# Performance work log

Hardware: AMD Instinct MI355X
Metric: run time of the kernel (lower is better)

## Reference

```python
import jax, jax.numpy as jnp
import numpy as np

HIDDEN = 1024
HEADS = 16
HEAD_DIM = HIDDEN // HEADS
NEG_INF = -1.0e9


def setup_inputs() -> dict:
    key = jax.random.key(0)
    ks = jax.random.split(key, 9)
    B, S = 4, 2048
    scale = 1.0 / np.sqrt(HIDDEN)
    inp = {
        'query': jax.random.normal(ks[0], (B, S, HIDDEN), dtype=jnp.float32),
        'masks': jnp.ones((B, S), dtype=jnp.float32),
        'Wq': jax.random.normal(ks[1], (HIDDEN, HIDDEN), dtype=jnp.float32) * scale,
        'bq': jnp.zeros((HIDDEN,), dtype=jnp.float32),
        'Wk': jax.random.normal(ks[2], (HIDDEN, HIDDEN), dtype=jnp.float32) * scale,
        'bk': jnp.zeros((HIDDEN,), dtype=jnp.float32),
        'Wv': jax.random.normal(ks[3], (HIDDEN, HIDDEN), dtype=jnp.float32) * scale,
        'bv': jnp.zeros((HIDDEN,), dtype=jnp.float32),
        'Wo': jax.random.normal(ks[4], (HIDDEN, HIDDEN), dtype=jnp.float32) * scale,
        'bo': jnp.zeros((HIDDEN,), dtype=jnp.float32),
    }
    return inp


def _split_heads(x):
    # [B, S, H*D] -> [B, H, S, D]
    B, S, C = x.shape
    return x.reshape(B, S, HEADS, C // HEADS).transpose(0, 2, 1, 3)


def reference(query, masks, Wq, bq, Wk, bk, Wv, bv, Wo, bo):
    # torch Linear: y = x @ W.T + b
    q = query @ Wq.T + bq
    k = query @ Wk.T + bk
    v = query @ Wv.T + bv
    qh = _split_heads(q) * (HEAD_DIM ** -0.5)  # [B,H,S,D]
    kh = _split_heads(k)
    vh = _split_heads(v)
    bias = ((1.0 - masks) * NEG_INF)[:, None, None, :]  # [B,1,1,S]
    logits = jnp.einsum('bhqd,bhkd->bhqk', qh, kh) + bias
    weights = jax.nn.softmax(logits, axis=-1)  # dropout p=0.0 -> identity
    x = jnp.einsum('bhqk,bhkd->bhqd', weights, vh)  # [B,H,S,D]
    B, H, S, D = x.shape
    combined = x.transpose(0, 2, 1, 3).reshape(B, S, H * D)
    return combined @ Wo.T + bo
```

## Files before the change

### kernel.cpp

```cpp
#include <hip/hip_runtime.h>

typedef unsigned short u16;
typedef unsigned int u32;
typedef u16 u16x4 __attribute__((ext_vector_type(4)));
typedef u16 u16x8 __attribute__((ext_vector_type(8)));
typedef u32 u32x4 __attribute__((ext_vector_type(4)));
typedef __bf16 bf16x8 __attribute__((ext_vector_type(8)));
typedef float f32x4 __attribute__((ext_vector_type(4)));

#define GPTR(p) (const __attribute__((address_space(1))) void*)(p)
#define LPTR(p) (__attribute__((address_space(3))) void*)(p)
#define ASYNC16(g, l) __builtin_amdgcn_global_load_lds(GPTR(g), LPTR(l), 16, 0, 0)

#if __has_builtin(__builtin_amdgcn_exp2f)
#define EXP2(x) __builtin_amdgcn_exp2f(x)
#else
#define EXP2(x) __builtin_exp2f(x)
#endif

__device__ __forceinline__ u16 f2bf(float f) {
    u32 u = __builtin_bit_cast(u32, f);
    return (u16)((u + 0x7fffu + ((u >> 16) & 1u)) >> 16);
}
__device__ __forceinline__ bf16x8 ld8(const void* p) {
    return __builtin_bit_cast(bf16x8, *(const u16x8*)p);
}

__global__ void cvt_all(const float* __restrict__ q,
                        const float* __restrict__ wq, const float* __restrict__ wk,
                        const float* __restrict__ wv, const float* __restrict__ wo,
                        u16* __restrict__ xb, u16* __restrict__ wcat, u16* __restrict__ wob) {
    const int blk = blockIdx.x;
    const float* src;
    u16* dst;
    size_t base;
    if (blk < 8192) {
        src = q; dst = xb; base = (size_t)blk * 256;
    } else {
        const int t = blk - 8192;
        const int w = t >> 10;
        base = (size_t)(t & 1023) * 256;
        src = (w == 0) ? wq : (w == 1) ? wk : (w == 2) ? wv : wo;
        dst = (w == 0) ? wcat : (w == 1) ? wcat + 1024 * 1024
            : (w == 2) ? wcat + 2 * 1024 * 1024 : wob;
    }
    const size_t i = base + threadIdx.x;
    float4 v = ((const float4*)src)[i];
    ushort4 o4;
    o4.x = f2bf(v.x); o4.y = f2bf(v.y); o4.z = f2bf(v.z); o4.w = f2bf(v.w);
    ((ushort4*)dst)[i] = o4;
}

template<int MODE>
__global__ __launch_bounds__(256, 2) void gemm_bt(
    const u16* __restrict__ A, const u16* __restrict__ B,
    const float* __restrict__ b0, const float* __restrict__ b1, const float* __restrict__ b2,
    u16* __restrict__ O0, u16* __restrict__ O1, u16* __restrict__ O2,
    float* __restrict__ OF)
{
    constexpr int K = 1024;
    constexpr int NBLK = (MODE == 0) ? 24 : 8;
    constexpr int CPX  = (MODE == 0) ? 192 : 64;
    __shared__ __align__(16) u16 As[128 * 32];
    __shared__ __align__(16) u16 Bs[128 * 32];
    const int tid = threadIdx.x;
    const int wave = tid >> 6, lane = tid & 63;
    const int lin = blockIdx.y * (int)gridDim.x + blockIdx.x;
    const int nl = (lin & 7) * CPX + (lin >> 3);
    const int m0 = (nl / NBLK) * 128, n0 = (nl % NBLK) * 128;
    const int wm = (wave >> 1) * 64, wn = (wave & 1) * 64;
    const int fr = lane & 15, fg = lane >> 4;

    f32x4 acc[4][4] = {};

    const int srow = lane >> 2;
    const int scol = (lane & 3) * 8;
    const u16* aSrc = A + (size_t)(m0 + wave * 32 + srow) * K + scol;
    const u16* bSrc = B + (size_t)(n0 + wave * 32 + srow) * K + scol;
    u16* const aDst0 = &As[(wave * 32) * 32];
    u16* const aDst1 = &As[(wave * 32 + 16) * 32];
    u16* const bDst0 = &Bs[(wave * 32) * 32];
    u16* const bDst1 = &Bs[(wave * 32 + 16) * 32];

    for (int kt = 0; kt < K; kt += 32) {
        ASYNC16(aSrc + kt,          aDst0);
        ASYNC16(aSrc + kt + 16 * K, aDst1);
        ASYNC16(bSrc + kt,          bDst0);
        ASYNC16(bSrc + kt + 16 * K, bDst1);
        __syncthreads();
        bf16x8 af[4], bfv[4];
        #pragma unroll
        for (int i = 0; i < 4; ++i) af[i]  = ld8(&As[(wm + i * 16 + fr) * 32 + fg * 8]);
        #pragma unroll
        for (int j = 0; j < 4; ++j) bfv[j] = ld8(&Bs[(wn + j * 16 + fr) * 32 + fg * 8]);
        #pragma unroll
        for (int i = 0; i < 4; ++i)
            #pragma unroll
            for (int j = 0; j < 4; ++j)
                acc[i][j] = __builtin_amdgcn_mfma_f32_16x16x32_bf16(af[i], bfv[j], acc[i][j], 0, 0, 0);
        __syncthreads();
    }

    if constexpr (MODE == 0) {
        const float QSCALE = 0.125f * 1.44269504f;
        #pragma unroll
        for (int j = 0; j < 4; ++j) {
            const int n = n0 + wn + j * 16 + fr;
            const int sel = n >> 10;
            const int w = n & 1023;
            const float bb = (sel == 0 ? b0 : sel == 1 ? b1 : b2)[w];
            const int h = w >> 6, d = w & 63;
            if (sel == 2) {
                #pragma unroll
                for (int i = 0; i < 4; ++i) {
                    const int m = m0 + wm + i * 16 + fg * 4;
                    u16x4 st;
                    #pragma unroll
                    for (int r = 0; r < 4; ++r) st[r] = f2bf(acc[i][j][r] + bb);
                    *(u16x4*)&O2[((size_t)(((m >> 11) * 16 + h) * 64 + d)) * 2048 + (m & 2047)] = st;
                }
            } else {
                const float scale = (sel == 0) ? QSCALE : 1.0f;
                u16* const dst = (sel == 0 ? O0 : O1);
                #pragma unroll
                for (int i = 0; i < 4; ++i) {
                    #pragma unroll
                    for (int r = 0; r < 4; ++r) {
                        const int m = m0 + wm + i * 16 + fg * 4 + r;
                        dst[(((size_t)((m >> 11) * 16 + h) * 2048 + (m & 2047)) << 6) + d] =
                            f2bf((acc[i][j][r] + bb) * scale);
                    }
                }
            }
        }
    } else {
        #pragma unroll
        for (int j = 0; j < 4; ++j) {
            const int n = n0 + wn + j * 16 + fr;
            const float bb = b0[n];
            #pragma unroll
            for (int i = 0; i < 4; ++i) {
                #pragma unroll
                for (int r = 0; r < 4; ++r) {
                    const int m = m0 + wm + i * 16 + fg * 4 + r;
                    OF[(size_t)m * 1024 + n] = acc[i][j][r] + bb;
                }
            }
        }
    }
}

template<bool MASKED>
__device__ __forceinline__ void kv_loop(
    char* smem, const u16* __restrict__ Kbh, const u16* __restrict__ Vtbh,
    const float* __restrict__ mrow, int wave, int fg, int a0, int a1, int t0,
    int srow, int scb, bf16x8 (&qf)[2][2], f32x4 (&o)[4][2], f32x4 (&den)[2],
    const f32x4& FZ, const bf16x8& ONES)
{
    auto STAGE = [&](int buf, int kv0) {
        #pragma unroll
        for (int j = 0; j < 2; ++j) {
            const int r0 = wave * 16 + j * 8;
            const int row = r0 + srow;
            const int sw = scb ^ ((row & 7) << 4);
            ASYNC16((const char*)(Kbh + (size_t)(kv0 + row) * 64) + sw,
                    smem + buf * 8192 + r0 * 128);
            ASYNC16((const char*)(Vtbh + (size_t)row * 2048 + kv0) + sw,
                    smem + 16384 + buf * 8192 + r0 * 128);
        }
    };

    STAGE(0, t0 * 64);
    for (int it = 0; it < 32; it += 2) {
        #pragma unroll
        for (int half = 0; half < 2; ++half) {
            const int tile = (t0 + it + half) & 31;
            const int kv = tile * 64;
            const int kb = half * 8192;
            const int vb = 16384 + half * 8192;
            __syncthreads();
            if (it + half < 31) STAGE(half ^ 1, ((tile + 1) & 31) * 64);

            float4 mv[4];
            if (MASKED) {
                #pragma unroll
                for (int nj = 0; nj < 4; ++nj)
                    mv[nj] = *(const float4*)(mrow + kv + nj * 16 + fg * 4);
            }

            #pragma unroll
            for (int hh = 0; hh < 2; ++hh) {
                const int aK = hh ? a1 : a0;
                f32x4 s[2][2];
                #pragma unroll
                for (int njl = 0; njl < 2; ++njl) {
                    const int nj = hh * 2 + njl;
                    bf16x8 k0 = ld8(smem + kb + nj * 2048 + a0);
                    bf16x8 k1 = ld8(smem + kb + nj * 2048 + a1);
                    __builtin_amdgcn_s_setprio(1);
                    #pragma unroll
                    for (int qs = 0; qs < 2; ++qs) {
                        f32x4 z = __builtin_amdgcn_mfma_f32_16x16x32_bf16(k0, qf[qs][0], FZ, 0, 0, 0);
                        s[njl][qs] = __builtin_amdgcn_mfma_f32_16x16x32_bf16(k1, qf[qs][1], z, 0, 0, 0);
                    }
                    __builtin_amdgcn_s_setprio(0);
                }
                #pragma unroll
                for (int njl = 0; njl < 2; ++njl) {
                    const int nj = hh * 2 + njl;
                    #pragma unroll
                    for (int qs = 0; qs < 2; ++qs)
                        #pragma unroll
                        for (int r = 0; r < 4; ++r) {
                            float p = EXP2(s[njl][qs][r]);
                            if (MASKED) p *= mv[nj][r];
                            s[njl][qs][r] = p;
                        }
                }
                bf16x8 pa[2];
                #pragma unroll
                for (int qs = 0; qs < 2; ++qs) {
                    u32 m0, m1, m2, m3;
                    asm("v_cvt_pk_bf16_f32 %0, %1, %2" : "=v"(m0) : "v"(s[0][qs][0]), "v"(s[0][qs][1]));
                    asm("v_cvt_pk_bf16_f32 %0, %1, %2" : "=v"(m1) : "v"(s[0][qs][2]), "v"(s[0][qs][3]));
                    asm("v_cvt_pk_bf16_f32 %0, %1, %2" : "=v"(m2) : "v"(s[1][qs][0]), "v"(s[1][qs][1]));
                    asm("v_cvt_pk_bf16_f32 %0, %1, %2" : "=v"(m3) : "v"(s[1][qs][2]), "v"(s[1][qs][3]));
                    asm("v_permlane32_swap_b32 %0, %1" : "+v"(m0), "+v"(m2));
                    asm("v_permlane32_swap_b32 %0, %1" : "+v"(m1), "+v"(m3));
                    asm("v_permlane16_swap_b32 %0, %1" : "+v"(m0), "+v"(m2));
                    asm("v_permlane16_swap_b32 %0, %1" : "+v"(m1), "+v"(m3));
                    pa[qs] = __builtin_bit_cast(bf16x8, u32x4{m0, m1, m2, m3});
                }

                __builtin_amdgcn_s_setprio(1);
                #pragma unroll
                for (int qs = 0; qs < 2; ++qs)
                    den[qs] = __builtin_amdgcn_mfma_f32_16x16x32_bf16(ONES, pa[qs], den[qs], 0, 0, 0);
                #pragma unroll
                for (int dj = 0; dj < 4; ++dj) {
                    bf16x8 v = ld8(smem + vb + dj * 2048 + aK);
                    #pragma unroll
                    for (int qs = 0; qs < 2; ++qs)
                        o[dj][qs] = __builtin_amdgcn_mfma_f32_16x16x32_bf16(v, pa[qs], o[dj][qs], 0, 0, 0);
                }
                __builtin_amdgcn_s_setprio(0);
            }
        }
    }
}

__global__ __launch_bounds__(256, 4) void attn_fwd(
    const u16* __restrict__ Qg, const u16* __restrict__ Kg, const u16* __restrict__ Vt,
    const float* __restrict__ masks, u16* __restrict__ X2)
{
    __shared__ __align__(16) char smem[32768];
    const int tid = threadIdx.x;
    const int wave = tid >> 6, lane = tid & 63;

    const int bidL = blockIdx.x;
    const int wg = ((bidL & 7) << 7) | (bidL >> 3);
    const int bh = wg >> 4;
    const int q0 = (wg & 15) * 128 + wave * 32;
    const int b = bh >> 4, h = bh & 15;
    const int fr = lane & 15, fg = lane >> 4;
    const int swz = (fr & 7) << 4;

    const int a0 = fr * 128 + ((fg * 16) ^ swz);
    const int a1 = fr * 128 + ((64 + fg * 16) ^ swz);

    const u16* const Kbh  = Kg + (size_t)bh * 2048 * 64;
    const u16* const Vtbh = Vt + (size_t)bh * 64 * 2048;
    const float* mrow = masks + b * 2048;

    bf16x8 qf[2][2];
    #pragma unroll
    for (int qs = 0; qs < 2; ++qs) {
        const u16* qp = Qg + ((size_t)bh * 2048 + q0 + qs * 16 + fr) * 64 + fg * 8;
        qf[qs][0] = ld8(qp);
        qf[qs][1] = ld8(qp + 32);
    }

    bool ok = true;
    {
        const float4* mp = (const float4*)mrow;
        #pragma unroll
        for (int i = 0; i < 8; ++i) {
            float4 m = mp[lane + i * 64];
            ok = ok && (m.x == 1.0f) && (m.y == 1.0f) && (m.z == 1.0f) && (m.w == 1.0f);
        }
        ok = __all(ok);
    }

    f32x4 o[4][2] = {};
    f32x4 den[2] = {};
    const f32x4 FZ = {0.f, 0.f, 0.f, 0.f};
    const u16x8 ONE_BITS = {0x3F80,0x3F80,0x3F80,0x3F80,0x3F80,0x3F80,0x3F80,0x3F80};
    const bf16x8 ONES = __builtin_bit_cast(bf16x8, ONE_BITS);

    const int srow = lane >> 3;
    const int scb = (lane & 7) * 16;

    const int t0 = (((bidL >> 8) & 3) << 3);

    if (ok)
        kv_loop<false>(smem, Kbh, Vtbh, mrow, wave, fg, a0, a1, t0, srow, scb,
                       qf, o, den, FZ, ONES);
    else
        kv_loop<true>(smem, Kbh, Vtbh, mrow, wave, fg, a0, a1, t0, srow, scb,
                      qf, o, den, FZ, ONES);

    #pragma unroll
    for (int qs = 0; qs < 2; ++qs) {
        const float inv = 1.0f / den[qs][0];
        const int q = q0 + qs * 16 + fr;
        u16* dst = X2 + ((size_t)(b * 2048 + q)) * 1024 + h * 64 + fg * 4;
        #pragma unroll
        for (int dj = 0; dj < 4; ++dj) {
            u16x4 st;
            #pragma unroll
            for (int r = 0; r < 4; ++r) st[r] = f2bf(o[dj][qs][r] * inv);
            *(u16x4*)(dst + dj * 16) = st;
        }
    }
}

extern "C" void kernel_launch(void* const* d_in, const int* in_sizes, int n_in,
                              void* d_out, int out_size, void* d_ws, size_t ws_size,
                              hipStream_t stream) {
    const float* query = (const float*)d_in[0];
    const float* masks = (const float*)d_in[1];
    const float* Wq = (const float*)d_in[2];
    const float* bq = (const float*)d_in[3];
    const float* Wk = (const float*)d_in[4];
    const float* bk = (const float*)d_in[5];
    const float* Wv = (const float*)d_in[6];
    const float* bv = (const float*)d_in[7];
    const float* Wo = (const float*)d_in[8];
    const float* bo = (const float*)d_in[9];
    float* out = (float*)d_out;

    char* ws = (char*)d_ws;
    u16* Xb   = (u16*)(ws);
    u16* Wcat = (u16*)(ws + (16u << 20));
    u16* Wob  = (u16*)(ws + (22u << 20));
    u16* Qg   = (u16*)(ws + (24u << 20));
    u16* Kg   = (u16*)(ws + (40u << 20));
    u16* Vt   = (u16*)(ws + (56u << 20));
    u16* X2   = Xb;

    cvt_all<<<12288, 256, 0, stream>>>(query, Wq, Wk, Wv, Wo, Xb, Wcat, Wob);
    gemm_bt<0><<<dim3(24, 64), 256, 0, stream>>>(Xb, Wcat, bq, bk, bv, Qg, Kg, Vt, nullptr);
    attn_fwd<<<1024, 256, 0, stream>>>(Qg, Kg, Vt, masks, X2);
    gemm_bt<1><<<dim3(8, 64), 256, 0, stream>>>(X2, Wob, bo, nullptr, nullptr, nullptr,
                                                nullptr, nullptr, out);
}
```

Before: 183.2 us.

## Double GEMM K-tile to 64 with XOR-swizzled LDS layout and higher occupancy

The projection GEMM now stages 64-wide K tiles instead of 32, halving the number of barrier pairs per K loop. Global-to-LDS async loads use an XOR swizzle on 16-byte chunks, and the fragment reads apply the matching swizzle to avoid LDS bank conflicts on the 128-byte rows. Launch bounds ask for 4 blocks per CU instead of 2. LDS use per block doubles, and the tighter register budget may cause spills.

```diff
diff --git a/kernel.cpp b/kernel.cpp
--- a/kernel.cpp
+++ b/kernel.cpp
@@ -52,7 +52,7 @@
 }
 
 template<int MODE>
-__global__ __launch_bounds__(256, 2) void gemm_bt(
+__global__ __launch_bounds__(256, 4) void gemm_bt(
     const u16* __restrict__ A, const u16* __restrict__ B,
     const float* __restrict__ b0, const float* __restrict__ b1, const float* __restrict__ b2,
     u16* __restrict__ O0, u16* __restrict__ O1, u16* __restrict__ O2,
@@ -61,8 +61,8 @@
     constexpr int K = 1024;
     constexpr int NBLK = (MODE == 0) ? 24 : 8;
     constexpr int CPX  = (MODE == 0) ? 192 : 64;
-    __shared__ __align__(16) u16 As[128 * 32];
-    __shared__ __align__(16) u16 Bs[128 * 32];
+    __shared__ __align__(16) u16 As[128 * 64];
+    __shared__ __align__(16) u16 Bs[128 * 64];
     const int tid = threadIdx.x;
     const int wave = tid >> 6, lane = tid & 63;
     const int lin = blockIdx.y * (int)gridDim.x + blockIdx.x;
@@ -73,31 +73,35 @@
 
     f32x4 acc[4][4] = {};
 
-    const int srow = lane >> 2;
-    const int scol = (lane & 3) * 8;
-    const u16* aSrc = A + (size_t)(m0 + wave * 32 + srow) * K + scol;
-    const u16* bSrc = B + (size_t)(n0 + wave * 32 + srow) * K + scol;
-    u16* const aDst0 = &As[(wave * 32) * 32];
-    u16* const aDst1 = &As[(wave * 32 + 16) * 32];
-    u16* const bDst0 = &Bs[(wave * 32) * 32];
-    u16* const bDst1 = &Bs[(wave * 32 + 16) * 32];
-
-    for (int kt = 0; kt < K; kt += 32) {
-        ASYNC16(aSrc + kt,          aDst0);
-        ASYNC16(aSrc + kt + 16 * K, aDst1);
-        ASYNC16(bSrc + kt,          bDst0);
-        ASYNC16(bSrc + kt + 16 * K, bDst1);
+    const int srow = lane >> 3;
+    const int sw = (((lane & 7) ^ srow) << 4);
+    const int rdo0 = (fg * 16) ^ ((fr & 7) << 4);
+    const int rdo1 = (64 + fg * 16) ^ ((fr & 7) << 4);
+
+    for (int kt = 0; kt < K; kt += 64) {
+        #pragma unroll
+        for (int j = 0; j < 4; ++j) {
+            const int row = wave * 32 + j * 8;
+            ASYNC16((const char*)(A + (size_t)(m0 + row + srow) * K + kt) + sw,
+                    (char*)As + row * 128);
+            ASYNC16((const char*)(B + (size_t)(n0 + row + srow) * K + kt) + sw,
+                    (char*)Bs + row * 128);
+        }
         __syncthreads();
-        bf16x8 af[4], bfv[4];
-        #pragma unroll
-        for (int i = 0; i < 4; ++i) af[i]  = ld8(&As[(wm + i * 16 + fr) * 32 + fg * 8]);
-        #pragma unroll
-        for (int j = 0; j < 4; ++j) bfv[j] = ld8(&Bs[(wn + j * 16 + fr) * 32 + fg * 8]);
-        #pragma unroll
-        for (int i = 0; i < 4; ++i)
-            #pragma unroll
-            for (int j = 0; j < 4; ++j)
-                acc[i][j] = __builtin_amdgcn_mfma_f32_16x16x32_bf16(af[i], bfv[j], acc[i][j], 0, 0, 0);
+        #pragma unroll
+        for (int half = 0; half < 2; ++half) {
+            const int co = half ? rdo1 : rdo0;
+            bf16x8 af[4], bfv[4];
+            #pragma unroll
+            for (int i = 0; i < 4; ++i) af[i]  = ld8((const char*)As + (wm + i * 16 + fr) * 128 + co);
+            #pragma unroll
+            for (int j = 0; j < 4; ++j) bfv[j] = ld8((const char*)Bs + (wn + j * 16 + fr) * 128 + co);
+            #pragma unroll
+            for (int i = 0; i < 4; ++i)
+                #pragma unroll
+                for (int j = 0; j < 4; ++j)
+                    acc[i][j] = __builtin_amdgcn_mfma_f32_16x16x32_bf16(af[i], bfv[j], acc[i][j], 0, 0, 0);
+        }
         __syncthreads();
     }
 
```

New measurement: 172.2 us. 6.0% less time.
